# Kernel optimization log

Hardware: AMD Instinct MI355X
Metric: run time of the kernel (lower is better)

The kernel has to match this reference:

```python
import jax, jax.numpy as jnp
import numpy as np

EPS = 1e-7  # keras backend epsilon
B, H, W, C = 16, 112, 112, 64
F, KS = 128, 3


def _stack3x3_same(image):
    # Faithful to SharpCosSim2D.stack3x3 with padding='same', stride=1:
    # zero-padded im2col, kernel offsets row-major, stacked on axis=3.
    b, h, w, c = image.shape
    pimg = jnp.pad(image, ((0, 0), (1, 1), (1, 1), (0, 0)))
    patches = jnp.stack(
        [pimg[:, di:di + h, dj:dj + w, :] for di in range(3) for dj in range(3)],
        axis=3,
    )  # (B, oy, ox, 9, C)
    return patches


def setup_inputs() -> dict:
    key = jax.random.key(0)
    k1, k2 = jax.random.split(key)
    image = jax.random.normal(k1, (B, H, W, C), jnp.float32)
    # glorot-ish scale for the kernel matrix (1, C*k^2, F)
    w = jax.random.normal(k2, (1, C * KS * KS, F), jnp.float32) * (1.0 / np.sqrt(C * KS * KS))
    b_ = jnp.zeros((F,), jnp.float32)   # bias_initializer='zeros'
    p = jnp.ones((F,), jnp.float32)     # sharpening exponent, init ones
    q = jnp.zeros((1,), jnp.float32)    # norm offset, init zeros
    return {"image": image, "w": w, "b": b_, "p": p, "q": q}


def reference(image, w, b, p, q):
    bsz, h, wd, c = image.shape
    x = _stack3x3_same(image)                       # (B, oy, ox, 9, C)
    oy, ox = x.shape[1], x.shape[2]
    x = x.reshape(bsz, oy * ox, KS * KS * c)        # (B, flat, 9*C)
    # l2_normal: sqrt(max(sum_sq, eps)); q^2 added as learnable norm offset
    x_norm = jnp.sqrt(jnp.maximum(jnp.sum(x * x, axis=2, keepdims=True), EPS)) + q * q
    w_norm = jnp.sqrt(jnp.maximum(jnp.sum(w * w, axis=1, keepdims=True), EPS))
    y = jnp.einsum('bnk,ukf->bnf', x / x_norm, w / w_norm)  # cosine sims (B, flat, F)
    sgn = jnp.sign(y)
    y = sgn * jnp.power(jnp.abs(y) + EPS, p * p) + b        # sharpen + bias
    return y.reshape(bsz, oy, ox, F)
```

## Files before the change

### kernel.cpp

```cpp
#include <hip/hip_runtime.h>
#include <hip/hip_bf16.h>

#define EPS 1e-7f

typedef __attribute__((ext_vector_type(8))) short short8;
typedef __attribute__((ext_vector_type(4))) float f32x4;

__device__ __forceinline__ short f2bf(float x) {
    __hip_bfloat16 h = __float2bfloat16(x);
    short r; __builtin_memcpy(&r, &h, 2); return r;
}

__device__ __forceinline__ float fast_log2(float x) {
    float r; asm("v_log_f32 %0, %1" : "=v"(r) : "v"(x)); return r;
}
__device__ __forceinline__ float fast_exp2(float x) {
    float r; asm("v_exp_f32 %0, %1" : "=v"(r) : "v"(x)); return r;
}

__global__ void prep_kernel(const float* __restrict__ w, const float* __restrict__ p,
                            short* __restrict__ Wn2, float* __restrict__ p2) {
    __shared__ float pn[4][128];
    __shared__ float sInv[128];
    const int t = blockIdx.x;
    const int tid = threadIdx.x;
    const int n = tid & 127, part = tid >> 7;
    float ssq = 0.f;
    const int k0 = part * 144;
    for (int k = k0; k < k0 + 144; ++k) {
        float v = w[k * 128 + n];
        ssq = fmaf(v, v, ssq);
    }
    pn[part][n] = ssq;
    __syncthreads();
    if (tid < 128) {
        float s = pn[0][tid] + pn[1][tid] + pn[2][tid] + pn[3][tid];
        sInv[tid] = 1.0f / sqrtf(fmaxf(s, EPS));
        if (t == 0) p2[tid] = p[tid] * p[tid];
    }
    __syncthreads();
    if (tid < 256) {
        const int mxl = tid & 15, g = (tid >> 4) & 7, ks = tid >> 7;
        const int nn = g * 16 + mxl;
        const float inv = sInv[nn];
        short* dst = Wn2 + (((t * 2 + ks) * 8 + g) * 16 + mxl) * 32;
        const float* src = w + (t * 64 + ks * 32) * 128 + nn;
#pragma unroll
        for (int j = 0; j < 32; ++j) dst[j] = f2bf(src[j * 128] * inv);
    }
}

__global__ __launch_bounds__(512, 4)
void sharp_main(const float* __restrict__ img, const short* __restrict__ Wn,
                const float* __restrict__ bias, const float* __restrict__ p2g,
                const float* __restrict__ qp, float* __restrict__ out) {
    __shared__ __align__(16) unsigned char lds_img[41472];
    __shared__ float sArr[324];
    __shared__ float invxn[256];

    const int tid  = threadIdx.x;
    const int lane = tid & 63;
    const int wv   = tid >> 6;
    const int wm   = wv >> 1;
    const int wn   = wv & 1;
    const int tx = blockIdx.x, ty = blockIdx.y, bz = blockIdx.z;
    const int y0 = ty * 16, x0 = tx * 16;

    const int mxl = lane & 15;
    const int kq  = lane >> 4;

    if (tid < 324) sArr[tid] = 0.f;
    __syncthreads();

    {
        const long ibase = (long)bz * (112 * 112 * 64);
        for (int q = tid; q < 2592; q += 512) {
            const int pp = q >> 3, c8 = q & 7;
            const int py = pp / 18, px = pp % 18;
            const int gy = y0 - 1 + py, gx = x0 - 1 + px;
            short8 h = {0, 0, 0, 0, 0, 0, 0, 0};
            if ((unsigned)gy < 112u && (unsigned)gx < 112u) {
                const float* sp = img + ibase + ((gy * 112 + gx) << 6) + (c8 << 3);
                const float4 v0 = *reinterpret_cast<const float4*>(sp);
                const float4 v1 = *reinterpret_cast<const float4*>(sp + 4);
                float ss = v0.x * v0.x + v0.y * v0.y + v0.z * v0.z + v0.w * v0.w
                         + v1.x * v1.x + v1.y * v1.y + v1.z * v1.z + v1.w * v1.w;
                h[0] = f2bf(v0.x); h[1] = f2bf(v0.y); h[2] = f2bf(v0.z); h[3] = f2bf(v0.w);
                h[4] = f2bf(v1.x); h[5] = f2bf(v1.y); h[6] = f2bf(v1.z); h[7] = f2bf(v1.w);
                atomicAdd(&sArr[pp], ss);
            }
            const int addr = (pp << 7) + (((c8 << 4)) ^ ((pp & 7) << 4));
            *reinterpret_cast<short8*>(lds_img + addr) = h;
        }
    }
    __syncthreads();

    if (tid < 256) {
        const int my = tid >> 4, mx = tid & 15;
        float s9 = 0.f;
#pragma unroll
        for (int dy = 0; dy < 3; ++dy)
#pragma unroll
            for (int dx = 0; dx < 3; ++dx)
                s9 += sArr[(my + dy) * 18 + (mx + dx)];
        const float qv = qp[0];
        invxn[tid] = 1.0f / (sqrtf(fmaxf(s9, EPS)) + qv * qv);
    }
    __syncthreads();

    f32x4 acc[4][4];
#pragma unroll
    for (int mi = 0; mi < 4; ++mi)
#pragma unroll
        for (int ni = 0; ni < 4; ++ni)
            acc[mi][ni] = (f32x4){0.f, 0.f, 0.f, 0.f};

#pragma unroll
    for (int t = 0; t < 9; ++t) {
        const int dy = t / 3, dx = t % 3;
#pragma unroll
        for (int ks = 0; ks < 2; ++ks) {
            short8 af[4], bfr[4];
#pragma unroll
            for (int ni = 0; ni < 4; ++ni) {
                const int off = ((((t * 2 + ks) * 8 + wn * 4 + ni) * 16 + mxl) * 32) + kq * 8;
                bfr[ni] = *reinterpret_cast<const short8*>(Wn + off);
            }
#pragma unroll
            for (int mi = 0; mi < 4; ++mi) {
                const int pp = (wm * 4 + mi + dy) * 18 + mxl + dx;
                const int addr = (pp << 7) + ((ks * 64 + kq * 16) ^ ((pp & 7) << 4));
                af[mi] = *reinterpret_cast<const short8*>(lds_img + addr);
            }
#pragma unroll
            for (int mi = 0; mi < 4; ++mi)
#pragma unroll
                for (int ni = 0; ni < 4; ++ni)
                    acc[mi][ni] = __builtin_amdgcn_mfma_f32_16x16x32_bf16(
                        af[mi], bfr[ni], acc[mi][ni], 0, 0, 0);
        }
    }

    float p2v[4], bv[4];
#pragma unroll
    for (int ni = 0; ni < 4; ++ni) {
        const int f = wn * 64 + ni * 16 + mxl;
        p2v[ni] = p2g[f];
        bv[ni] = bias[f];
    }
    const long obase = (long)bz * 112 * 112 * 128;
#pragma unroll
    for (int mi = 0; mi < 4; ++mi) {
        const int my = wm * 4 + mi;
        const int gy = y0 + my;
#pragma unroll
        for (int j = 0; j < 4; ++j) {
            const int mx = kq * 4 + j;
            const float inv = invxn[my * 16 + mx];
            const int gx = x0 + mx;
            float* op = out + obase + ((long)(gy * 112 + gx) << 7);
#pragma unroll
            for (int ni = 0; ni < 4; ++ni) {
                const float cosv = acc[mi][ni][j] * inv;
                const float av = fabsf(cosv) + EPS;
                const float r = fast_exp2(p2v[ni] * fast_log2(av));
                const float val = (cosv == 0.f) ? bv[ni] : (copysignf(r, cosv) + bv[ni]);
                op[wn * 64 + ni * 16 + mxl] = val;
            }
        }
    }
}

extern "C" void kernel_launch(void* const* d_in, const int* in_sizes, int n_in,
                              void* d_out, int out_size, void* d_ws, size_t ws_size,
                              hipStream_t stream) {
    const float* img = (const float*)d_in[0];
    const float* w   = (const float*)d_in[1];
    const float* b   = (const float*)d_in[2];
    const float* p   = (const float*)d_in[3];
    const float* q   = (const float*)d_in[4];
    float* out = (float*)d_out;

    short* Wn = (short*)d_ws;
    float* p2 = (float*)((char*)d_ws + 9 * 8192 * 2);

    prep_kernel<<<9, 512, 0, stream>>>(w, p, Wn, p2);
    sharp_main<<<dim3(7, 7, 16), 512, 0, stream>>>(img, Wn, b, p2, q, out);
}
```

Before: 251.3 us.

## Stage weights in double-buffered LDS and swap MFMA operands for vector stores

Weights are re-laid out as [tap][filter][k] and staged per tap into a swizzled, double-buffered LDS region, with the next tap prefetched from global into registers. This replaces per-wave direct global loads of B fragments. MFMA operand order is swapped so each lane holds four consecutive filters for one pixel, which allows float4 output stores and vector loads of bias and p². The cost is 32KB of extra LDS, which may reduce occupancy, plus a barrier per tap.

```diff
diff --git a/kernel.cpp b/kernel.cpp
--- a/kernel.cpp
+++ b/kernel.cpp
@@ -19,7 +19,7 @@
 }
 
 __global__ void prep_kernel(const float* __restrict__ w, const float* __restrict__ p,
-                            short* __restrict__ Wn2, float* __restrict__ p2) {
+                            short* __restrict__ Wn, float* __restrict__ p2) {
     __shared__ float pn[4][128];
     __shared__ float sInv[128];
     const int t = blockIdx.x;
@@ -40,11 +40,10 @@
     }
     __syncthreads();
     if (tid < 256) {
-        const int mxl = tid & 15, g = (tid >> 4) & 7, ks = tid >> 7;
-        const int nn = g * 16 + mxl;
+        const int nn = tid & 127, kh = tid >> 7;
         const float inv = sInv[nn];
-        short* dst = Wn2 + (((t * 2 + ks) * 8 + g) * 16 + mxl) * 32;
-        const float* src = w + (t * 64 + ks * 32) * 128 + nn;
+        short* dst = Wn + t * 8192 + nn * 64 + kh * 32;
+        const float* src = w + (t * 64 + kh * 32) * 128 + nn;
 #pragma unroll
         for (int j = 0; j < 32; ++j) dst[j] = f2bf(src[j * 128] * inv);
     }
@@ -55,6 +54,7 @@
                 const float* __restrict__ bias, const float* __restrict__ p2g,
                 const float* __restrict__ qp, float* __restrict__ out) {
     __shared__ __align__(16) unsigned char lds_img[41472];
+    __shared__ __align__(16) unsigned char lds_w[2][16384];
     __shared__ float sArr[324];
     __shared__ float invxn[256];
 
@@ -93,6 +93,16 @@
             *reinterpret_cast<short8*>(lds_img + addr) = h;
         }
     }
+
+    const uint4* wg = reinterpret_cast<const uint4*>(Wn);
+    const int wi0 = tid * 2, wi1 = tid * 2 + 1;
+    const int wa0 = (tid * 32) ^ ((((tid * 32) >> 7) & 7) << 4);
+    const int wa1 = (tid * 32 + 16) ^ ((((tid * 32) >> 7) & 7) << 4);
+    uint4 r0 = wg[wi0], r1 = wg[wi1];
+    *reinterpret_cast<uint4*>(lds_w[0] + wa0) = r0;
+    *reinterpret_cast<uint4*>(lds_w[0] + wa1) = r1;
+    r0 = wg[1024 + wi0]; r1 = wg[1024 + wi1];
+
     __syncthreads();
 
     if (tid < 256) {
@@ -118,13 +128,19 @@
 #pragma unroll
     for (int t = 0; t < 9; ++t) {
         const int dy = t / 3, dx = t % 3;
+        if (t < 8) {
+            *reinterpret_cast<uint4*>(lds_w[(t + 1) & 1] + wa0) = r0;
+            *reinterpret_cast<uint4*>(lds_w[(t + 1) & 1] + wa1) = r1;
+            if (t < 7) { r0 = wg[(t + 2) * 1024 + wi0]; r1 = wg[(t + 2) * 1024 + wi1]; }
+        }
 #pragma unroll
         for (int ks = 0; ks < 2; ++ks) {
-            short8 af[4], bfr[4];
+            short8 wf[4], af[4];
 #pragma unroll
             for (int ni = 0; ni < 4; ++ni) {
-                const int off = ((((t * 2 + ks) * 8 + wn * 4 + ni) * 16 + mxl) * 32) + kq * 8;
-                bfr[ni] = *reinterpret_cast<const short8*>(Wn + off);
+                const int nn = wn * 64 + ni * 16 + mxl;
+                const int addr = (nn << 7) + ((ks * 64 + kq * 16) ^ ((nn & 7) << 4));
+                wf[ni] = *reinterpret_cast<const short8*>(lds_w[t & 1] + addr);
             }
 #pragma unroll
             for (int mi = 0; mi < 4; ++mi) {
@@ -137,36 +153,36 @@
 #pragma unroll
                 for (int ni = 0; ni < 4; ++ni)
                     acc[mi][ni] = __builtin_amdgcn_mfma_f32_16x16x32_bf16(
-                        af[mi], bfr[ni], acc[mi][ni], 0, 0, 0);
-        }
-    }
-
-    float p2v[4], bv[4];
+                        wf[ni], af[mi], acc[mi][ni], 0, 0, 0);
+        }
+        __syncthreads();
+    }
+
+    f32x4 p2v[4], bv[4];
 #pragma unroll
     for (int ni = 0; ni < 4; ++ni) {
-        const int f = wn * 64 + ni * 16 + mxl;
-        p2v[ni] = p2g[f];
-        bv[ni] = bias[f];
+        const int f0 = wn * 64 + ni * 16 + kq * 4;
+        p2v[ni] = *reinterpret_cast<const f32x4*>(p2g + f0);
+        bv[ni]  = *reinterpret_cast<const f32x4*>(bias + f0);
     }
     const long obase = (long)bz * 112 * 112 * 128;
 #pragma unroll
     for (int mi = 0; mi < 4; ++mi) {
         const int my = wm * 4 + mi;
         const int gy = y0 + my;
-#pragma unroll
-        for (int j = 0; j < 4; ++j) {
-            const int mx = kq * 4 + j;
-            const float inv = invxn[my * 16 + mx];
-            const int gx = x0 + mx;
-            float* op = out + obase + ((long)(gy * 112 + gx) << 7);
-#pragma unroll
-            for (int ni = 0; ni < 4; ++ni) {
+        const float inv = invxn[my * 16 + mxl];
+        float* op = out + obase + ((long)(gy * 112 + x0 + mxl) << 7);
+#pragma unroll
+        for (int ni = 0; ni < 4; ++ni) {
+            f32x4 v;
+#pragma unroll
+            for (int j = 0; j < 4; ++j) {
                 const float cosv = acc[mi][ni][j] * inv;
                 const float av = fabsf(cosv) + EPS;
-                const float r = fast_exp2(p2v[ni] * fast_log2(av));
-                const float val = (cosv == 0.f) ? bv[ni] : (copysignf(r, cosv) + bv[ni]);
-                op[wn * 64 + ni * 16 + mxl] = val;
-            }
+                const float r = fast_exp2(p2v[ni][j] * fast_log2(av));
+                v[j] = (cosv == 0.f) ? bv[ni][j] : (copysignf(r, cosv) + bv[ni][j]);
+            }
+            *reinterpret_cast<f32x4*>(op + wn * 64 + ni * 16 + kq * 4) = v;
         }
     }
 }
```

Measured after the change: 226.5 us. 1.11x faster.
